# Performance work log

Measured on AMD Instinct MI355X. Metric: run time of the kernel, lower is better.

## Reference

```python
import jax, jax.numpy as jnp
import numpy as np


def setup_inputs() -> dict:
    key = jax.random.key(0)
    k1, k2, k3 = jax.random.split(key, 3)
    B, IN, H, OUT = 2048, 4096, 4096, 1024
    x = jax.random.normal(k1, (B, IN), dtype=jnp.float32)
    fc1_weight = jax.random.randint(k2, (H, IN), 0, 2).astype(jnp.int32)
    fc2_weight = jax.random.randint(k3, (OUT, H), 0, 2).astype(jnp.int32)
    return {"x": x, "fc1_weight": fc1_weight, "fc2_weight": fc2_weight, "threshold": 2048}


def _binary_popcount_matmul(a, w):
    # a: (B, K) in {0,1}, w: (N, K) in {0,1}
    # matches = sum_k 1 - (a XOR w) = a@w.T + (1-a)@(1-w).T  (identical math,
    # avoids materializing the (B, N, K) XNOR tensor the naive code builds)
    return jnp.einsum('bk,nk->bn', a, w) + jnp.einsum('bk,nk->bn', 1 - a, 1 - w)


def reference(x, fc1_weight, fc2_weight, threshold):
    xb = (x.reshape(x.shape[0], -1) >= 0).astype(jnp.int32)   # binarize input
    pc1 = _binary_popcount_matmul(xb, fc1_weight)              # (B, H) popcounts
    act1 = (pc1 >= threshold).astype(jnp.int32)                # threshold activation
    pc2 = _binary_popcount_matmul(act1, fc2_weight)            # (B, OUT) popcounts
    return pc2
```

## Files before the change

kernel.cpp:

```cpp
#include <hip/hip_runtime.h>
#include <stdint.h>

typedef int v4i  __attribute__((ext_vector_type(4)));
typedef int v16i __attribute__((ext_vector_type(16)));

__device__ __forceinline__ void gload_lds16(const void* g, void* l) {
    __builtin_amdgcn_global_load_lds(
        (const __attribute__((address_space(1))) void*)g,
        (__attribute__((address_space(3))) void*)l, 16, 0, 0);
}

template<typename T, bool ISFLOAT>
__global__ __launch_bounds__(512)
void pack_frag(const T* __restrict__ in, int8_t* __restrict__ F, int K) {
    __shared__ int8_t lbuf[32 * 1040];
    const int t  = threadIdx.x;
    const int db = blockIdx.y;
    const int c0 = blockIdx.x << 10;

    #pragma unroll
    for (int p = 0; p < 16; ++p) {
        int idx = p * 512 + t;
        int row = idx >> 8, c4 = idx & 255;
        uint32_t b;
        if constexpr (ISFLOAT) {
            const float4 v = *(const float4*)(in + (size_t)(db * 32 + row) * K + c0 + c4 * 4);
            b =  (v.x >= 0.0f ? 0x01u : 0xFFu)
              | ((v.y >= 0.0f ? 0x01u : 0xFFu) << 8)
              | ((v.z >= 0.0f ? 0x01u : 0xFFu) << 16)
              | ((v.w >= 0.0f ? 0x01u : 0xFFu) << 24);
        } else {
            const int4 v = *(const int4*)(in + (size_t)(db * 32 + row) * K + c0 + c4 * 4);
            b =  (v.x ? 0x01u : 0xFFu)
              | ((v.y ? 0x01u : 0xFFu) << 8)
              | ((v.z ? 0x01u : 0xFFu) << 16)
              | ((v.w ? 0x01u : 0xFFu) << 24);
        }
        *(uint32_t*)(lbuf + row * 1040 + c4 * 4) = b;
    }
    __syncthreads();

    const int s  = t >> 4;
    const int l0 = (t & 15) * 4;
    const int KC = K >> 5;
    int8_t* dst = F + ((size_t)db * KC + blockIdx.x * 32 + s) * 1024;
    #pragma unroll
    for (int li = 0; li < 4; ++li) {
        int l = l0 + li;
        uint4 v = *(const uint4*)(lbuf + (l & 31) * 1040 + s * 32 + (l >> 5) * 16);
        *(uint4*)(dst + l * 16) = v;
    }
}

__global__ __launch_bounds__(256, 2)
void bnn_l1_areg(const int8_t* __restrict__ Af,
                 const int8_t* __restrict__ Bf,
                 const int* __restrict__ thr_ptr,
                 int8_t* __restrict__ actf)
{
    constexpr int KC  = 128;
    constexpr int NKT = 64;
    constexpr uint32_t BUFSZ = 8192;

    __shared__ int8_t lds[3 * 8192];

    const int tid  = threadIdx.x;
    const int lane = tid & 63;
    const int wv   = tid >> 6;
    const int wr   = wv >> 1, wc = wv & 1;

    const int g   = blockIdx.x;
    const int idx = g >> 3;
    const int bn  = (g & 7) * 4 + (idx >> 4);
    const int bm  = idx & 15;

    const int8_t* gB0; const int8_t* gB1;
    uint32_t lo0, lo1;
    {
        int s0 = tid;
        gB0 = Bf + ((size_t)(bn * 4 + (s0 >> 7)) * KC + ((s0 >> 6) & 1)) * 1024 + (s0 & 63) * 16;
        lo0 = (uint32_t)s0 * 16;
        int s1 = tid + 256;
        gB1 = Bf + ((size_t)(bn * 4 + (s1 >> 7)) * KC + ((s1 >> 6) & 1)) * 1024 + (s1 & 63) * 16;
        lo1 = (uint32_t)s1 * 16;
    }

    const int8_t* gA = Af + ((size_t)(bm * 4 + wr * 2) * KC) * 1024 + lane * 16;

    v16i acc[2][2];
    #pragma unroll
    for (int i = 0; i < 2; ++i)
        #pragma unroll
        for (int j = 0; j < 2; ++j) acc[i][j] = {};

    v4i aA0 = *(const v4i*)(gA);
    v4i aA1 = *(const v4i*)(gA + 1024);
    v4i aA2 = *(const v4i*)(gA + 131072);
    v4i aA3 = *(const v4i*)(gA + 132096);
    gload_lds16(gB0, lds + lo0);         gB0 += 2048;
    gload_lds16(gB1, lds + lo1);         gB1 += 2048;
    gload_lds16(gB0, lds + BUFSZ + lo0); gB0 += 2048;
    gload_lds16(gB1, lds + BUFSZ + lo1); gB1 += 2048;
    v4i aB0{}, aB1{}, aB2{}, aB3{};

    uint32_t bo = 0;

    auto kt_body = [&](int kt, v4i& AR0, v4i& AR1, v4i& AR2, v4i& AR3,
                               v4i& AW0, v4i& AW1, v4i& AW2, v4i& AW3) {
        if (kt + 1 < NKT) asm volatile("s_waitcnt vmcnt(2)" ::: "memory");
        else              asm volatile("s_waitcnt vmcnt(0)" ::: "memory");
        __builtin_amdgcn_sched_barrier(0);
        __builtin_amdgcn_s_barrier();
        __builtin_amdgcn_sched_barrier(0);

        const uint32_t sbo = (bo >= BUFSZ) ? (bo - BUFSZ) : (2u * BUFSZ);
        const int8_t* Bb = lds + bo + wc * 4096 + lane * 16;

        v4i bf00 = *(const v4i*)(Bb + 0);
        v4i bf10 = *(const v4i*)(Bb + 2048);
        __builtin_amdgcn_s_setprio(1);
        acc[0][0] = __builtin_amdgcn_mfma_i32_32x32x32_i8(AR0, bf00, acc[0][0], 0, 0, 0);
        acc[0][1] = __builtin_amdgcn_mfma_i32_32x32x32_i8(AR0, bf10, acc[0][1], 0, 0, 0);
        acc[1][0] = __builtin_amdgcn_mfma_i32_32x32x32_i8(AR2, bf00, acc[1][0], 0, 0, 0);
        acc[1][1] = __builtin_amdgcn_mfma_i32_32x32x32_i8(AR2, bf10, acc[1][1], 0, 0, 0);
        __builtin_amdgcn_s_setprio(0);

        if (kt + 1 < NKT) {
            const int8_t* ga = gA + (kt + 1) * 2048;
            AW0 = *(const v4i*)(ga);
            AW1 = *(const v4i*)(ga + 1024);
            AW2 = *(const v4i*)(ga + 131072);
            AW3 = *(const v4i*)(ga + 132096);
            __builtin_amdgcn_sched_barrier(0);
        }
        if (kt + 2 < NKT) {
            gload_lds16(gB0, lds + sbo + lo0); gB0 += 2048;
            gload_lds16(gB1, lds + sbo + lo1); gB1 += 2048;
        }

        v4i bf01 = *(const v4i*)(Bb + 1024);
        v4i bf11 = *(const v4i*)(Bb + 3072);
        __builtin_amdgcn_s_setprio(1);
        acc[0][0] = __builtin_amdgcn_mfma_i32_32x32x32_i8(AR1, bf01, acc[0][0], 0, 0, 0);
        acc[0][1] = __builtin_amdgcn_mfma_i32_32x32x32_i8(AR1, bf11, acc[0][1], 0, 0, 0);
        acc[1][0] = __builtin_amdgcn_mfma_i32_32x32x32_i8(AR3, bf01, acc[1][0], 0, 0, 0);
        acc[1][1] = __builtin_amdgcn_mfma_i32_32x32x32_i8(AR3, bf11, acc[1][1], 0, 0, 0);
        __builtin_amdgcn_s_setprio(0);

        bo = (bo == 2u * BUFSZ) ? 0u : bo + BUFSZ;
    };

    #pragma unroll 1
    for (int kt = 0; kt < NKT; kt += 2) {
        kt_body(kt,     aA0, aA1, aA2, aA3, aB0, aB1, aB2, aB3);
        kt_body(kt + 1, aB0, aB1, aB2, aB3, aA0, aA1, aA2, aA3);
    }

    __syncthreads();
    const int thr = *thr_ptr;
    int8_t* bits = lds;
    #pragma unroll
    for (int i = 0; i < 2; ++i)
        #pragma unroll
        for (int j = 0; j < 2; ++j) {
            int dimb = wr * 64 + i * 32 + 4 * (lane >> 5);
            int gcl  = wc * 64 + j * 32 + (lane & 31);
            #pragma unroll
            for (int reg = 0; reg < 16; ++reg) {
                int dl = dimb + (reg & 3) + 8 * (reg >> 2);
                int match = (4096 + acc[i][j][reg]) >> 1;
                bits[dl * 144 + gcl] = (match >= thr) ? (int8_t)1 : (int8_t)-1;
            }
        }
    __syncthreads();
    const int s    = tid >> 4;
    const int dblk = s >> 2, kcl = s & 3;
    const int l0   = (tid & 15) * 4;
    int8_t* dst = actf + ((size_t)(bm * 4 + dblk) * KC + bn * 4 + kcl) * 1024;
    #pragma unroll
    for (int li = 0; li < 4; ++li) {
        int l = l0 + li;
        uint4 v = *(const uint4*)(bits + (dblk * 32 + (l & 31)) * 144
                                       + kcl * 32 + (l >> 5) * 16);
        *(uint4*)(dst + l * 16) = v;
    }
}

template<int WN>
__global__ __launch_bounds__(256, 1)
void bnn_mfma2(const int8_t* __restrict__ Af,
               const int8_t* __restrict__ Bf,
               int* __restrict__ out, int Nout)
{
    constexpr int KC     = 128;
    constexpr int NKT    = 64;
    constexpr int NBB    = 2 * WN;
    constexpr int ASLOTS = 512;
    constexpr int BSLOTS = 128 * NBB;
    constexpr int SLOTS  = ASLOTS + BSLOTS;
    constexpr int NLD    = SLOTS / 256;
    constexpr uint32_t BUFSZ = (uint32_t)SLOTS * 16;

    __shared__ int8_t lds[3][SLOTS * 16];

    const int tid  = threadIdx.x;
    const int lane = tid & 63;
    const int wv   = tid >> 6;
    const int wr   = wv >> 1, wc = wv & 1;

    const int g   = blockIdx.x;
    const int idx = g >> 3;
    const int bn  = (g & 7) * 2 + (idx >> 4);
    const int bm  = idx & 15;

    const int8_t* gsrc[NLD];
    uint32_t ldoff[NLD];
    #pragma unroll
    for (int i = 0; i < NLD; ++i) {
        int sbase = wv * 64 + 256 * i;
        ldoff[i] = (uint32_t)sbase * 16;
        const int8_t* base;
        if (sbase < ASLOTS) {
            int R = sbase >> 7, C = (sbase >> 6) & 1;
            base = Af + ((size_t)(bm * 4 + R) * KC + C) * 1024;
        } else {
            int s = sbase - ASLOTS;
            int R = s >> 7, C = (s >> 6) & 1;
            base = Bf + ((size_t)(bn * NBB + R) * KC + C) * 1024;
        }
        gsrc[i] = base + lane * 16;
    }

    auto stage = [&](int buf) {
        #pragma unroll
        for (int i = 0; i < NLD; ++i) {
            gload_lds16(gsrc[i], (int8_t*)lds + (uint32_t)buf * BUFSZ + ldoff[i]);
            gsrc[i] += 2048;
        }
    };

    v16i acc[2][WN];
    #pragma unroll
    for (int i = 0; i < 2; ++i)
        #pragma unroll
        for (int j = 0; j < WN; ++j) acc[i][j] = {};

    stage(0);
    stage(1);

    int cur = 0, nxt = 2;
    #pragma unroll 1
    for (int kt = 0; kt < NKT; ++kt) {
        if (kt < NKT - 1) asm volatile("s_waitcnt vmcnt(3)" ::: "memory");
        else              asm volatile("s_waitcnt vmcnt(0)" ::: "memory");
        __builtin_amdgcn_sched_barrier(0);
        __builtin_amdgcn_s_barrier();
        __builtin_amdgcn_sched_barrier(0);

        if (kt < NKT - 2) {
            stage(nxt);
            nxt = (nxt == 2) ? 0 : nxt + 1;
        }

        const int8_t* Al = lds[cur];
        const int8_t* Bl = lds[cur] + ASLOTS * 16;
        #pragma unroll
        for (int kc = 0; kc < 2; ++kc) {
            v4i af[2], bf[WN];
            #pragma unroll
            for (int i = 0; i < 2; ++i)
                af[i] = *(const v4i*)(Al + (((wr * 2 + i) * 2 + kc) * 64 + lane) * 16);
            #pragma unroll
            for (int j = 0; j < WN; ++j)
                bf[j] = *(const v4i*)(Bl + (((wc * WN + j) * 2 + kc) * 64 + lane) * 16);
            #pragma unroll
            for (int i = 0; i < 2; ++i)
                #pragma unroll
                for (int j = 0; j < WN; ++j)
                    acc[i][j] = __builtin_amdgcn_mfma_i32_32x32x32_i8(af[i], bf[j], acc[i][j], 0, 0, 0);
        }
        cur = (cur == 2) ? 0 : cur + 1;
    }

    #pragma unroll
    for (int i = 0; i < 2; ++i)
        #pragma unroll
        for (int j = 0; j < WN; ++j) {
            int gc = bn * (64 * WN) + wc * (32 * WN) + j * 32 + (lane & 31);
            #pragma unroll
            for (int reg = 0; reg < 16; ++reg) {
                int gr = bm * 128 + wr * 64 + i * 32
                       + (reg & 3) + 8 * (reg >> 2) + 4 * (lane >> 5);
                out[(size_t)gr * Nout + gc] = (4096 + acc[i][j][reg]) >> 1;
            }
        }
}

extern "C" void kernel_launch(void* const* d_in, const int* in_sizes, int n_in,
                              void* d_out, int out_size, void* d_ws, size_t ws_size,
                              hipStream_t stream) {
    const float* x   = (const float*)d_in[0];
    const int*   w1  = (const int*)d_in[1];
    const int*   w2  = (const int*)d_in[2];
    const int*   thr = (const int*)d_in[3];
    int* out = (int*)d_out;

    const int B = 2048, IN = 4096, H = 4096, OUT = 1024;
    uint8_t* ws = (uint8_t*)d_ws;

    int8_t* Af  = (int8_t*)(ws);
    int8_t* W1f = (int8_t*)(ws + ((size_t)8  << 20));
    int8_t* W2f = (int8_t*)(ws + ((size_t)24 << 20));
    int8_t* Act = (int8_t*)(ws + ((size_t)28 << 20));

    pack_frag<float, true ><<<dim3(IN / 1024, B   / 32), 512, 0, stream>>>(x,  Af,  IN);
    pack_frag<int,   false><<<dim3(IN / 1024, H   / 32), 512, 0, stream>>>(w1, W1f, IN);
    pack_frag<int,   false><<<dim3(H  / 1024, OUT / 32), 512, 0, stream>>>(w2, W2f, H);

    bnn_l1_areg<<<512, 256, 0, stream>>>(Af, W1f, thr, Act);
    bnn_mfma2<1><<<256, 256, 0, stream>>>(Act, W2f, out, OUT);
}
```

Baseline: 92.07 us.

## Deepen layer-1 main loop pipeline to four stages with asm global loads

Replaces the 3-buffer/2-register-set ping-pong in the layer-1 GEMM loop with a 4-stage pipeline: four LDS buffers for B and four register sets for A, with loads issued three k-tiles ahead. A loads use inline asm so vmcnt waits can be counted precisely, and all four B fragment LDS reads are issued before the eight MFMAs. The aim is to hide more global-memory latency. In exchange it uses more LDS (32KB) and more VGPRs, which may hurt occupancy under launch_bounds(256,2), and the waitcnt accounting is fragile.

```diff
diff --git a/kernel.cpp b/kernel.cpp
--- a/kernel.cpp
+++ b/kernel.cpp
@@ -8,6 +8,12 @@
     __builtin_amdgcn_global_load_lds(
         (const __attribute__((address_space(1))) void*)g,
         (__attribute__((address_space(3))) void*)l, 16, 0, 0);
+}
+
+__device__ __forceinline__ v4i gload16(const int8_t* p) {
+    v4i r;
+    asm volatile("global_load_dwordx4 %0, %1, off" : "=v"(r) : "v"(p) : "memory");
+    return r;
 }
 
 template<typename T, bool ISFLOAT>
@@ -60,9 +66,8 @@
 {
     constexpr int KC  = 128;
     constexpr int NKT = 64;
-    constexpr uint32_t BUFSZ = 8192;
-
-    __shared__ int8_t lds[3 * 8192];
+
+    __shared__ int8_t lds[4 * 8192];
 
     const int tid  = threadIdx.x;
     const int lane = tid & 63;
@@ -93,68 +98,66 @@
         #pragma unroll
         for (int j = 0; j < 2; ++j) acc[i][j] = {};
 
-    v4i aA0 = *(const v4i*)(gA);
-    v4i aA1 = *(const v4i*)(gA + 1024);
-    v4i aA2 = *(const v4i*)(gA + 131072);
-    v4i aA3 = *(const v4i*)(gA + 132096);
-    gload_lds16(gB0, lds + lo0);         gB0 += 2048;
-    gload_lds16(gB1, lds + lo1);         gB1 += 2048;
-    gload_lds16(gB0, lds + BUFSZ + lo0); gB0 += 2048;
-    gload_lds16(gB1, lds + BUFSZ + lo1); gB1 += 2048;
-    v4i aB0{}, aB1{}, aB2{}, aB3{};
-
-    uint32_t bo = 0;
-
-    auto kt_body = [&](int kt, v4i& AR0, v4i& AR1, v4i& AR2, v4i& AR3,
-                               v4i& AW0, v4i& AW1, v4i& AW2, v4i& AW3) {
-        if (kt + 1 < NKT) asm volatile("s_waitcnt vmcnt(2)" ::: "memory");
-        else              asm volatile("s_waitcnt vmcnt(0)" ::: "memory");
-        __builtin_amdgcn_sched_barrier(0);
-        __builtin_amdgcn_s_barrier();
-        __builtin_amdgcn_sched_barrier(0);
-
-        const uint32_t sbo = (bo >= BUFSZ) ? (bo - BUFSZ) : (2u * BUFSZ);
-        const int8_t* Bb = lds + bo + wc * 4096 + lane * 16;
-
-        v4i bf00 = *(const v4i*)(Bb + 0);
-        v4i bf10 = *(const v4i*)(Bb + 2048);
-        __builtin_amdgcn_s_setprio(1);
-        acc[0][0] = __builtin_amdgcn_mfma_i32_32x32x32_i8(AR0, bf00, acc[0][0], 0, 0, 0);
-        acc[0][1] = __builtin_amdgcn_mfma_i32_32x32x32_i8(AR0, bf10, acc[0][1], 0, 0, 0);
-        acc[1][0] = __builtin_amdgcn_mfma_i32_32x32x32_i8(AR2, bf00, acc[1][0], 0, 0, 0);
-        acc[1][1] = __builtin_amdgcn_mfma_i32_32x32x32_i8(AR2, bf10, acc[1][1], 0, 0, 0);
-        __builtin_amdgcn_s_setprio(0);
-
-        if (kt + 1 < NKT) {
-            const int8_t* ga = gA + (kt + 1) * 2048;
-            AW0 = *(const v4i*)(ga);
-            AW1 = *(const v4i*)(ga + 1024);
-            AW2 = *(const v4i*)(ga + 131072);
-            AW3 = *(const v4i*)(ga + 132096);
-            __builtin_amdgcn_sched_barrier(0);
-        }
-        if (kt + 2 < NKT) {
-            gload_lds16(gB0, lds + sbo + lo0); gB0 += 2048;
-            gload_lds16(gB1, lds + sbo + lo1); gB1 += 2048;
-        }
-
-        v4i bf01 = *(const v4i*)(Bb + 1024);
-        v4i bf11 = *(const v4i*)(Bb + 3072);
-        __builtin_amdgcn_s_setprio(1);
-        acc[0][0] = __builtin_amdgcn_mfma_i32_32x32x32_i8(AR1, bf01, acc[0][0], 0, 0, 0);
-        acc[0][1] = __builtin_amdgcn_mfma_i32_32x32x32_i8(AR1, bf11, acc[0][1], 0, 0, 0);
-        acc[1][0] = __builtin_amdgcn_mfma_i32_32x32x32_i8(AR3, bf01, acc[1][0], 0, 0, 0);
-        acc[1][1] = __builtin_amdgcn_mfma_i32_32x32x32_i8(AR3, bf11, acc[1][1], 0, 0, 0);
-        __builtin_amdgcn_s_setprio(0);
-
-        bo = (bo == 2u * BUFSZ) ? 0u : bo + BUFSZ;
-    };
+    v4i Ab[4][4];
+
+    #pragma unroll
+    for (int p = 0; p < 3; ++p) {
+        const int8_t* ga = gA + p * 2048;
+        Ab[p][0] = gload16(ga);
+        Ab[p][1] = gload16(ga + 1024);
+        Ab[p][2] = gload16(ga + 131072);
+        Ab[p][3] = gload16(ga + 132096);
+        gload_lds16(gB0, lds + p * 8192 + lo0); gB0 += 2048;
+        gload_lds16(gB1, lds + p * 8192 + lo1); gB1 += 2048;
+    }
+
+#define KT_BODY(KT, P)                                                         \
+    {                                                                          \
+        const int kt_ = (KT);                                                  \
+        if (kt_ < NKT - 2)      asm volatile("s_waitcnt vmcnt(12)" ::: "memory"); \
+        else if (kt_ == NKT - 2) asm volatile("s_waitcnt vmcnt(6)"  ::: "memory"); \
+        else                     asm volatile("s_waitcnt vmcnt(0)"  ::: "memory"); \
+        __builtin_amdgcn_sched_barrier(0);                                     \
+        __builtin_amdgcn_s_barrier();                                          \
+        __builtin_amdgcn_sched_barrier(0);                                     \
+        const int8_t* Bb = lds + (P) * 8192 + wc * 4096 + lane * 16;           \
+        v4i bf00 = *(const v4i*)(Bb + 0);                                      \
+        v4i bf10 = *(const v4i*)(Bb + 2048);                                   \
+        v4i bf01 = *(const v4i*)(Bb + 1024);                                   \
+        v4i bf11 = *(const v4i*)(Bb + 3072);                                   \
+        if (kt_ + 3 < NKT) {                                                   \
+            const int8_t* ga = gA + (kt_ + 3) * 2048;                          \
+            Ab[((P)+3)&3][0] = gload16(ga);                                    \
+            Ab[((P)+3)&3][1] = gload16(ga + 1024);                             \
+            Ab[((P)+3)&3][2] = gload16(ga + 131072);                           \
+            Ab[((P)+3)&3][3] = gload16(ga + 132096);                           \
+            gload_lds16(gB0, lds + (((P)+3)&3) * 8192 + lo0); gB0 += 2048;     \
+            gload_lds16(gB1, lds + (((P)+3)&3) * 8192 + lo1); gB1 += 2048;     \
+        }                                                                      \
+        __builtin_amdgcn_sched_barrier(0);                                     \
+        asm volatile("s_waitcnt lgkmcnt(0)" ::: "memory");                     \
+        __builtin_amdgcn_sched_barrier(0);                                     \
+        __builtin_amdgcn_s_setprio(1);                                         \
+        acc[0][0] = __builtin_amdgcn_mfma_i32_32x32x32_i8(Ab[P][0], bf00, acc[0][0], 0, 0, 0); \
+        acc[0][1] = __builtin_amdgcn_mfma_i32_32x32x32_i8(Ab[P][0], bf10, acc[0][1], 0, 0, 0); \
+        acc[1][0] = __builtin_amdgcn_mfma_i32_32x32x32_i8(Ab[P][2], bf00, acc[1][0], 0, 0, 0); \
+        acc[1][1] = __builtin_amdgcn_mfma_i32_32x32x32_i8(Ab[P][2], bf10, acc[1][1], 0, 0, 0); \
+        acc[0][0] = __builtin_amdgcn_mfma_i32_32x32x32_i8(Ab[P][1], bf01, acc[0][0], 0, 0, 0); \
+        acc[0][1] = __builtin_amdgcn_mfma_i32_32x32x32_i8(Ab[P][1], bf11, acc[0][1], 0, 0, 0); \
+        acc[1][0] = __builtin_amdgcn_mfma_i32_32x32x32_i8(Ab[P][3], bf01, acc[1][0], 0, 0, 0); \
+        acc[1][1] = __builtin_amdgcn_mfma_i32_32x32x32_i8(Ab[P][3], bf11, acc[1][1], 0, 0, 0); \
+        __builtin_amdgcn_s_setprio(0);                                         \
+        __builtin_amdgcn_sched_barrier(0);                                     \
+    }
 
     #pragma unroll 1
-    for (int kt = 0; kt < NKT; kt += 2) {
-        kt_body(kt,     aA0, aA1, aA2, aA3, aB0, aB1, aB2, aB3);
-        kt_body(kt + 1, aB0, aB1, aB2, aB3, aA0, aA1, aA2, aA3);
-    }
+    for (int kt0 = 0; kt0 < NKT; kt0 += 4) {
+        KT_BODY(kt0 + 0, 0)
+        KT_BODY(kt0 + 1, 1)
+        KT_BODY(kt0 + 2, 2)
+        KT_BODY(kt0 + 3, 3)
+    }
+#undef KT_BODY
 
     __syncthreads();
     const int thr = *thr_ptr;
```

After: 91.43 us. Within noise of the previous version (-0.7%).
